# Optimization experiments

Hardware: AMD Instinct MI355X
Metric: run time of the kernel (lower is better)

Reference implementation:

```python
import jax, jax.numpy as jnp
import numpy as np

B, S, D, H, FF, V, L = 2, 2048, 1024, 16, 4096, 32000, 4
HD = D // H
SCALE = HD ** -0.5
STD = 0.02


def _ln(x, w, b, eps=1e-5):
    mu = jnp.mean(x, axis=-1, keepdims=True)
    var = jnp.mean(jnp.square(x - mu), axis=-1, keepdims=True)
    return (x - mu) * jax.lax.rsqrt(var + eps) * w + b


def setup_inputs() -> dict:
    key = jax.random.key(0)
    ks = iter(jax.random.split(key, 16))

    def w(k, shape):
        return jax.random.normal(k, shape, jnp.float32) * STD

    inp = {
        "tokens": jax.random.randint(next(ks), (B, S), 0, V, jnp.int32),
        "tok_emb": w(next(ks), (V, D)),
        "ln_e_w": jnp.ones((D,), jnp.float32),
        "ln_e_b": jnp.zeros((D,), jnp.float32),
        "ln1_w": jnp.ones((L, D), jnp.float32),
        "ln1_b": jnp.zeros((L, D), jnp.float32),
        "wq": w(next(ks), (L, D, D)),
        "bq": jnp.zeros((L, D), jnp.float32),
        "wk": w(next(ks), (L, D, D)),
        "bk": jnp.zeros((L, D), jnp.float32),
        "wv": w(next(ks), (L, D, D)),
        "bv": jnp.zeros((L, D), jnp.float32),
        "wo": w(next(ks), (L, D, D)),
        "bo": jnp.zeros((L, D), jnp.float32),
        "ln2_w": jnp.ones((L, D), jnp.float32),
        "ln2_b": jnp.zeros((L, D), jnp.float32),
        "w1": w(next(ks), (L, D, 2 * FF)),
        "b1": jnp.zeros((L, 2 * FF), jnp.float32),
        "w2": w(next(ks), (L, FF, D)),
        "b2": jnp.zeros((L, D), jnp.float32),
        "lnf_w": jnp.ones((D,), jnp.float32),
        "lnf_b": jnp.zeros((D,), jnp.float32),
        "w_out": w(next(ks), (D, V)),
        "b_out": jnp.zeros((V,), jnp.float32),
    }
    return inp


def reference(tokens, tok_emb, ln_e_w, ln_e_b, ln1_w, ln1_b, wq, bq, wk, bk,
              wv, bv, wo, bo, ln2_w, ln2_b, w1, b1, w2, b2, lnf_w, lnf_b,
              w_out, b_out):
    x = tok_emb[tokens]                      # [B,S,D]
    x = _ln(x, ln_e_w, ln_e_b)               # embedding LayerNorm (dropout off)
    for l in range(L):
        # pre-LN attention
        h = _ln(x, ln1_w[l], ln1_b[l])
        q = (h @ wq[l] + bq[l]).reshape(B, S, H, HD)
        k = (h @ wk[l] + bk[l]).reshape(B, S, H, HD)
        v = (h @ wv[l] + bv[l]).reshape(B, S, H, HD)
        scores = jnp.einsum('bqhd,bkhd->bhqk', q, k) * SCALE
        attn = jax.nn.softmax(scores, axis=-1)
        o = jnp.einsum('bhqk,bkhd->bqhd', attn, v).reshape(B, S, D)
        x = x + (o @ wo[l] + bo[l])
        # pre-LN gated (GeGLU) FFN
        h = _ln(x, ln2_w[l], ln2_b[l])
        gv = h @ w1[l] + b1[l]               # [B,S,2*FF]
        gate, val = gv[..., :FF], gv[..., FF:]
        ff = jax.nn.gelu(gate, approximate=False) * val
        x = x + (ff @ w2[l] + b2[l])
    x = _ln(x, lnf_w, lnf_b)
    return x @ w_out + b_out                 # logits [B,S,V]
```

## Files before the change

### kernel.cpp

```cpp
#include <hip/hip_runtime.h>

typedef __attribute__((ext_vector_type(8))) short s16x8;
typedef __attribute__((ext_vector_type(4))) short s16x4;
typedef __attribute__((ext_vector_type(4))) float f32x4;

__device__ __forceinline__ unsigned short f2bf(float f){
    union{float f;unsigned u;}v; v.f=f;
    unsigned u=v.u;
    unsigned r=(u+0x7fffu+((u>>16)&1u))>>16;
    return (unsigned short)r;
}
__device__ __forceinline__ float bf2f(unsigned short s){
    union{unsigned u;float f;}v; v.u=((unsigned)s)<<16; return v.f;
}
__device__ __forceinline__ unsigned pk2t(float a, float b){
    return (__float_as_uint(a)>>16) | (__float_as_uint(b) & 0xffff0000u);
}
__device__ __forceinline__ unsigned pk2r(float a, float b){
    return (unsigned)f2bf(a) | ((unsigned)f2bf(b)<<16);
}
__device__ __forceinline__ f32x4 fmax4(f32x4 a, f32x4 b){
    f32x4 r; r[0]=fmaxf(a[0],b[0]); r[1]=fmaxf(a[1],b[1]);
    r[2]=fmaxf(a[2],b[2]); r[3]=fmaxf(a[3],b[3]); return r;
}

__device__ __forceinline__ void gl16(const void* g, void* l){
    __builtin_amdgcn_global_load_lds(
        (const __attribute__((address_space(1))) void*)g,
        (__attribute__((address_space(3))) void*)l, 16, 0, 0);
}

#define ATT_SCALE 0.125f

__global__ __launch_bounds__(256) void flash_k(
    const unsigned short* __restrict__ qkv,
    const unsigned short* __restrict__ vt,
    unsigned short* __restrict__ o)
{
    __shared__ __align__(16) unsigned short Pl[4][2048];
    const int t=threadIdx.x, w=t>>6, lane=t&63;
    const int lr=lane&15, lg=lane>>4;
    const int zb=blockIdx.y>>4, zh=blockIdx.y&15;
    const long sr0 = (long)zb*2048 + blockIdx.x*128 + w*32;
    const unsigned short* qb    = qkv + sr0*3072 + zh*64;
    const unsigned short* kbase = qkv + ((long)zb*2048)*3072 + 1024 + zh*64;
    const unsigned short* vtb   = vt + (long)zb*2097152 + (long)zh*131072;

    s16x8 qf[2][2];
    #pragma unroll
    for(int qg=0;qg<2;qg++)
        #pragma unroll
        for(int kc=0;kc<2;kc++)
            qf[qg][kc] = *(const s16x8*)(qb + (qg*16+lr)*3072 + kc*32 + lg*8);

    float m0=-1e30f, m1=-1e30f, l0=0.f, l1=0.f;
    f32x4 oa[2][4];
    #pragma unroll
    for(int qg=0;qg<2;qg++)
        #pragma unroll
        for(int dt=0;dt<4;dt++) oa[qg][dt]=f32x4{0.f,0.f,0.f,0.f};

    char* Pw = (char*)&Pl[w][0];
    const int swz = (lr&7)<<4;

    for(int kv0=0; kv0<2048; kv0+=64){
        f32x4 s[2][4];
        __builtin_amdgcn_s_setprio(1);
        #pragma unroll
        for(int kb=0;kb<4;kb++){
            const unsigned short* kr = kbase + (long)(kv0+kb*16+lr)*3072;
            s16x8 a0 = *(const s16x8*)(kr + lg*8);
            s16x8 a1 = *(const s16x8*)(kr + 32 + lg*8);
            #pragma unroll
            for(int qg=0;qg<2;qg++){
                f32x4 z4{0.f,0.f,0.f,0.f};
                z4 = __builtin_amdgcn_mfma_f32_16x16x32_bf16(a0, qf[qg][0], z4,0,0,0);
                s[qg][kb] = __builtin_amdgcn_mfma_f32_16x16x32_bf16(a1, qf[qg][1], z4,0,0,0);
            }
        }
        __builtin_amdgcn_s_setprio(0);
        s16x8 vreg[4][2];
        #pragma unroll
        for(int dt=0;dt<4;dt++){
            const unsigned short* vr = vtb + (dt*16+lr)*2048 + kv0;
            vreg[dt][0] = *(const s16x8*)(vr + lg*8);
            vreg[dt][1] = *(const s16x8*)(vr + 32 + lg*8);
        }
        #pragma unroll
        for(int qg=0;qg<2;qg++){
            float& m = qg? m1:m0;
            float& l = qg? l1:l0;
            f32x4 mx4 = fmax4(fmax4(s[qg][0],s[qg][1]),fmax4(s[qg][2],s[qg][3]));
            float bm = fmaxf(fmaxf(mx4[0],mx4[1]),fmaxf(mx4[2],mx4[3]));
            bm = fmaxf(bm, __shfl_xor(bm,16));
            bm = fmaxf(bm, __shfl_xor(bm,32));
            const float mn = fmaxf(m, bm);
            const float sc = __expf((m-mn)*ATT_SCALE);
            m = mn;
            float rs=0.f;
            #pragma unroll
            for(int kb=0;kb<4;kb++){
                f32x4 p;
                #pragma unroll
                for(int r=0;r<4;r++){ p[r]=__expf((s[qg][kb][r]-mn)*ATT_SCALE); rs+=p[r]; }
                s[qg][kb]=p;
            }
            rs += __shfl_xor(rs,16);
            rs += __shfl_xor(rs,32);
            l = l*sc + rs;
            #pragma unroll
            for(int dt=0;dt<4;dt++) oa[qg][dt] = oa[qg][dt]*sc;
            #pragma unroll
            for(int kb=0;kb<4;kb++){
                uint2 pw;
                pw.x = pk2t(s[qg][kb][0], s[qg][kb][1]);
                pw.y = pk2t(s[qg][kb][2], s[qg][kb][3]);
                *(uint2*)(Pw + (qg*16+lr)*128 + ((kb*32+lg*8)^swz)) = pw;
            }
        }
        asm volatile("s_waitcnt lgkmcnt(0)" ::: "memory");
        s16x8 pb0[2], pb1[2];
        #pragma unroll
        for(int qg=0;qg<2;qg++){
            pb0[qg] = *(const s16x8*)(Pw + (qg*16+lr)*128 + ((     lg*16)^swz));
            pb1[qg] = *(const s16x8*)(Pw + (qg*16+lr)*128 + ((64 + lg*16)^swz));
        }
        __builtin_amdgcn_s_setprio(1);
        #pragma unroll
        for(int dt=0;dt<4;dt++){
            #pragma unroll
            for(int qg=0;qg<2;qg++){
                oa[qg][dt] = __builtin_amdgcn_mfma_f32_16x16x32_bf16(vreg[dt][0], pb0[qg], oa[qg][dt],0,0,0);
                oa[qg][dt] = __builtin_amdgcn_mfma_f32_16x16x32_bf16(vreg[dt][1], pb1[qg], oa[qg][dt],0,0,0);
            }
        }
        __builtin_amdgcn_s_setprio(0);
    }
    #pragma unroll
    for(int qg=0;qg<2;qg++){
        const float inv = 1.f/(qg? l1:l0);
        #pragma unroll
        for(int dt=0;dt<4;dt++){
            uint2 st;
            st.x = pk2r(oa[qg][dt][0]*inv, oa[qg][dt][1]*inv);
            st.y = pk2r(oa[qg][dt][2]*inv, oa[qg][dt][3]*inv);
            *(uint2*)(o + (sr0+qg*16+lr)*1024 + zh*64 + dt*16 + lg*4) = st;
        }
    }
}

template<bool OBF16,bool BIAS,bool GEGLU>
__global__ __launch_bounds__(512,2) void gemm8_k(
    const unsigned short* __restrict__ A,
    const unsigned short* __restrict__ B,
    const float* __restrict__ bias,
    void* __restrict__ Cp,
    int K,int lda,int ldb,int ldc)
{
    __shared__ __align__(16) char lds[131072];
    const int t=threadIdx.x, w=t>>6, lane=t&63;
    const int wr=w>>2, wc=w&3;
    const int lr=lane&15, lg=lane>>4;

    const int nwg = gridDim.x*gridDim.y;
    const int id  = blockIdx.y*gridDim.x + blockIdx.x;
    const int nid = (id&7)*(nwg>>3) + (id>>3);
    const long row0 = (long)(nid % gridDim.x)*256;
    const long col0 = (long)(nid / gridDim.x)*256;

    const int NT = K>>6;

    const int csw0 = (lg*16) ^ ((lr&7)<<4);
    const int aRow = (wr*64+lr)*128;
    const int bRow = (wc*32+lr)*128;

    const int sro = t>>3;
    const int sce = (((t&7) ^ ((t>>3)&7))<<3);

#define STAGE(gp, ld_, lb) do{ \
    const unsigned short* _g=(gp); char* _l=(lb); \
    gl16(_g + (long)sro*(ld_) + sce, _l + t*16); \
    gl16(_g + (long)(sro+64)*(ld_) + sce, _l + 8192 + t*16); }while(0)

#define LDA8(m,kk) (*(const s16x8*)(Ab_ + aRow + ((m)&3)*2048 + ((m)>>2)*16384 + ((kk)? (csw0^64):csw0)))
#define LDB8(n,kk) (*(const s16x8*)(Bb_ + bRow + ((n)&1)*2048 + ((n)>>1)*16384 + ((kk)? (csw0^64):csw0)))

    f32x4 acc[8][4];
    #pragma unroll
    for(int m=0;m<8;m++)
        #pragma unroll
        for(int n=0;n<4;n++) acc[m][n]=f32x4{0.f,0.f,0.f,0.f};

    STAGE(A + row0*lda,        lda, lds);
    STAGE(B + col0*ldb,        ldb, lds+65536);
    STAGE(A + (row0+128)*lda,  lda, lds+16384);
    STAGE(B + (col0+128)*ldb,  ldb, lds+65536+16384);
    STAGE(A + row0*lda + 64,   lda, lds+32768);
    STAGE(B + col0*ldb + 64,   ldb, lds+65536+32768);
    asm volatile("s_waitcnt vmcnt(4)" ::: "memory");
    __builtin_amdgcn_s_barrier();

    for(int tt=0; tt<NT; ++tt){
        char* Ab_ = lds + ((tt&1)<<15);
        char* Bb_ = lds + 65536 + ((tt&1)<<15);
        char* An  = lds + (((tt+1)&1)<<15);
        char* Bn  = lds + 65536 + (((tt+1)&1)<<15);
        const int k1=(tt+1)<<6, k2=(tt+2)<<6;
        s16x8 a[4][2], b01[2][2], b23[2][2];

        #pragma unroll
        for(int m=0;m<4;m++){ a[m][0]=LDA8(m,0); a[m][1]=LDA8(m,1); }
        #pragma unroll
        for(int n=0;n<2;n++){ b01[n][0]=LDB8(n,0); b01[n][1]=LDB8(n,1); }
        if(tt+1<NT) STAGE(A + (row0+128)*lda + k1, lda, An+16384);
        __builtin_amdgcn_s_barrier();
        __builtin_amdgcn_s_setprio(1);
        #pragma unroll
        for(int kk=0;kk<2;kk++)
            #pragma unroll
            for(int m=0;m<4;m++)
                #pragma unroll
                for(int n=0;n<2;n++)
                    acc[m][n]=__builtin_amdgcn_mfma_f32_16x16x32_bf16(a[m][kk],b01[n][kk],acc[m][n],0,0,0);
        __builtin_amdgcn_s_setprio(0);
        __builtin_amdgcn_s_barrier();

        #pragma unroll
        for(int n=0;n<2;n++){ b23[n][0]=LDB8(n+2,0); b23[n][1]=LDB8(n+2,1); }
        if(tt+1<NT) STAGE(B + (col0+128)*ldb + k1, ldb, Bn+16384);
        __builtin_amdgcn_s_barrier();
        __builtin_amdgcn_s_setprio(1);
        #pragma unroll
        for(int kk=0;kk<2;kk++)
            #pragma unroll
            for(int m=0;m<4;m++)
                #pragma unroll
                for(int n=0;n<2;n++)
                    acc[m][n+2]=__builtin_amdgcn_mfma_f32_16x16x32_bf16(a[m][kk],b23[n][kk],acc[m][n+2],0,0,0);
        __builtin_amdgcn_s_setprio(0);
        __builtin_amdgcn_s_barrier();

        #pragma unroll
        for(int m=0;m<4;m++){ a[m][0]=LDA8(m+4,0); a[m][1]=LDA8(m+4,1); }
        if(tt+2<NT) STAGE(A + row0*lda + k2, lda, Ab_);
        __builtin_amdgcn_s_barrier();
        __builtin_amdgcn_s_setprio(1);
        #pragma unroll
        for(int kk=0;kk<2;kk++)
            #pragma unroll
            for(int m=0;m<4;m++)
                #pragma unroll
                for(int n=0;n<2;n++)
                    acc[m+4][n]=__builtin_amdgcn_mfma_f32_16x16x32_bf16(a[m][kk],b01[n][kk],acc[m+4][n],0,0,0);
        __builtin_amdgcn_s_setprio(0);
        __builtin_amdgcn_s_barrier();

        if(tt+2<NT) STAGE(B + col0*ldb + k2, ldb, Bb_);
        __builtin_amdgcn_s_barrier();
        __builtin_amdgcn_s_setprio(1);
        #pragma unroll
        for(int kk=0;kk<2;kk++)
            #pragma unroll
            for(int m=0;m<4;m++)
                #pragma unroll
                for(int n=0;n<2;n++)
                    acc[m+4][n+2]=__builtin_amdgcn_mfma_f32_16x16x32_bf16(a[m][kk],b23[n][kk],acc[m+4][n+2],0,0,0);
        __builtin_amdgcn_s_setprio(0);
        if(tt+2<NT) asm volatile("s_waitcnt vmcnt(4)" ::: "memory");
        else        asm volatile("s_waitcnt vmcnt(0)" ::: "memory");
        __builtin_amdgcn_s_barrier();
    }

    if constexpr(GEGLU){
        const long hc0 = col0>>1;
        #pragma unroll
        for(int m=0;m<8;m++){
            #pragma unroll
            for(int n=0;n<2;n++){
                #pragma unroll
                for(int rr=0;rr<4;rr++){
                    const long grow = row0 + wr*64 + (m&3)*16 + (m>>2)*128 + lg*4 + rr;
                    const long g    = hc0 + wc*32 + n*16 + lr;
                    float gg = acc[m][n][rr]   + bias[g];
                    float vl = acc[m][n+2][rr] + bias[4096+g];
                    float ge = 0.5f*gg*(1.f+erff(gg*0.70710678118654752f));
                    ((unsigned short*)Cp)[grow*(long)ldc + g] = f2bf(ge*vl);
                }
            }
        }
    } else if constexpr(!OBF16){
        float* L = (float*)lds;
        const int lc4 = (t&63)*4;
        f32x4 bv{0.f,0.f,0.f,0.f};
        if constexpr(BIAS) bv = *(const f32x4*)(bias + col0 + lc4);
        #pragma unroll
        for(int ch=0; ch<2; ch++){
            __builtin_amdgcn_s_barrier();
            #pragma unroll
            for(int mm=0;mm<4;mm++){
                #pragma unroll
                for(int n=0;n<4;n++){
                    #pragma unroll
                    for(int rr=0;rr<4;rr++){
                        const int lrow = wr*64 + mm*16 + lg*4 + rr;
                        const int lcol = wc*32 + (n&1)*16 + (n>>1)*128 + lr;
                        L[lrow*256 + lcol] = acc[ch*4+mm][n][rr];
                    }
                }
            }
            __builtin_amdgcn_s_barrier();
            #pragma unroll
            for(int p=0;p<16;p++){
                const int lrow = p*8 + (t>>6);
                f32x4 v4 = *(const f32x4*)(L + lrow*256 + lc4);
                if constexpr(BIAS){ v4[0]+=bv[0]; v4[1]+=bv[1]; v4[2]+=bv[2]; v4[3]+=bv[3]; }
                *(f32x4*)((float*)Cp + (row0 + ch*128 + lrow)*(long)ldc + col0 + lc4) = v4;
            }
        }
    } else {
        #pragma unroll
        for(int m=0;m<8;m++){
            #pragma unroll
            for(int n=0;n<4;n++){
                #pragma unroll
                for(int rr=0;rr<4;rr++){
                    const long grow = row0 + wr*64 + (m&3)*16 + (m>>2)*128 + lg*4 + rr;
                    const long gcol = col0 + wc*32 + (n&1)*16 + (n>>1)*128 + lr;
                    float vv = acc[m][n][rr];
                    if constexpr(BIAS) vv += bias[gcol];
                    ((unsigned short*)Cp)[grow*(long)ldc+gcol]=f2bf(vv);
                }
            }
        }
    }
#undef STAGE
#undef LDA8
#undef LDB8
}

__global__ __launch_bounds__(256) void cat3_k(const float* __restrict__ a,
    const float* __restrict__ b, const float* __restrict__ c,
    float* __restrict__ out)
{
    const int i = blockIdx.x*256+threadIdx.x;
    const int l = i/3072, cc = i%3072;
    float v = (cc<1024)? a[l*1024+cc] : (cc<2048)? b[l*1024+cc-1024] : c[l*1024+cc-2048];
    out[i]=v;
}

template<int BM,int BN,int WN,bool BIAS,bool RES,bool OBF16,bool SCL,bool SWAP,bool GEGLU>
__global__ __launch_bounds__(256) void gemm_bt(
    const unsigned short* __restrict__ A,
    const unsigned short* __restrict__ B,
    const unsigned short* __restrict__ B2,
    const float* __restrict__ bias,
    const float* __restrict__ res,
    void* __restrict__ Cp,
    int K,int lda,int ldb,int ldc,
    long aSb,long aSh,long bSb,long bSh,long cSb,long cSh,int zH)
{
    constexpr int BK=64;
    constexpr int WM=4/WN, WTM=BM/WM, WTN=BN/WN;
    constexpr int FM=WTM/16, FN=WTN/16;
    constexpr int CA=BM/8, CB=BN/8;
    __shared__ __align__(16) unsigned short As[BM*BK];
    __shared__ __align__(16) unsigned short Bs[BN*BK*(GEGLU?2:1)];

    const int t=threadIdx.x, w=t>>6, lane=t&63;
    const int wr=w/WN, wc=w%WN;
    const int lr=lane&15, lg=lane>>4;
    const int z=blockIdx.z, zb=z/zH, zh=z%zH;
    const long row0 = SWAP ? (long)blockIdx.x*BM : (long)blockIdx.y*BM;
    const long col0 = SWAP ? (long)blockIdx.y*BN : (long)blockIdx.x*BN;

    const unsigned short* Ab = A + zb*aSb + zh*aSh;
    const unsigned short* Bb = B + zb*bSb + zh*bSh;

    const int lr8 = lane>>3;
    const int lc8 = (lane&7)<<3;

    f32x4 acc[FM][FN];
    f32x4 acc2[GEGLU?FM:1][GEGLU?FN:1];
    #pragma unroll
    for(int i=0;i<FM;i++)
        #pragma unroll
        for(int j=0;j<FN;j++){
            acc[i][j]=f32x4{0.f,0.f,0.f,0.f};
            if constexpr(GEGLU) acc2[i][j]=f32x4{0.f,0.f,0.f,0.f};
        }

    const int NT=K/BK;
    for(int kt=0;kt<NT;kt++){
        const int kb=kt*BK;
        #pragma unroll
        for(int cc=0;cc<CA/4;cc++){
            const int c=cc*4+w;
            gl16(Ab + (row0 + c*8 + lr8)*(long)lda + kb + lc8, (char*)As + c*1024);
        }
        #pragma unroll
        for(int cc=0;cc<CB/4;cc++){
            const int c=cc*4+w;
            gl16(Bb + (col0 + c*8 + lr8)*(long)ldb + kb + lc8, (char*)Bs + c*1024);
        }
        if constexpr(GEGLU){
            #pragma unroll
            for(int cc=0;cc<CB/4;cc++){
                const int c=cc*4+w;
                gl16(B2 + (col0 + c*8 + lr8)*(long)ldb + kb + lc8,
                     (char*)Bs + (CB + c)*1024);
            }
        }
        __syncthreads();
        const unsigned short* Arp = As + (wr*WTM+lr)*BK + lg*8;
        const unsigned short* Brp = Bs + (wc*WTN+lr)*BK + lg*8;
        #pragma unroll
        for(int kk=0;kk<2;kk++){
            s16x8 af[FM], bfv[FN], bf2[GEGLU?FN:1];
            #pragma unroll
            for(int i=0;i<FM;i++) af[i] = *(const s16x8*)(Arp + i*16*BK + kk*32);
            #pragma unroll
            for(int j=0;j<FN;j++) bfv[j]= *(const s16x8*)(Brp + j*16*BK + kk*32);
            if constexpr(GEGLU){
                #pragma unroll
                for(int j=0;j<FN;j++) bf2[j]=*(const s16x8*)(Brp + BN*BK + j*16*BK + kk*32);
            }
            #pragma unroll
            for(int i=0;i<FM;i++)
                #pragma unroll
                for(int j=0;j<FN;j++){
                    acc[i][j]=__builtin_amdgcn_mfma_f32_16x16x32_bf16(af[i],bfv[j],acc[i][j],0,0,0);
                    if constexpr(GEGLU)
                        acc2[i][j]=__builtin_amdgcn_mfma_f32_16x16x32_bf16(af[i],bf2[j],acc2[i][j],0,0,0);
                }
        }
        __syncthreads();
    }
    #pragma unroll
    for(int i=0;i<FM;i++){
        #pragma unroll
        for(int j=0;j<FN;j++){
            #pragma unroll
            for(int r=0;r<4;r++){
                const long grow = row0 + wr*WTM + i*16 + lg*4 + r;
                const long gcol = col0 + wc*WTN + j*16 + lr;
                if constexpr(GEGLU){
                    float g  = acc[i][j][r]  + bias[gcol];
                    float vl = acc2[i][j][r] + bias[gcol+4096];
                    float ge = 0.5f*g*(1.f+erff(g*0.70710678118654752f));
                    ((unsigned short*)Cp)[grow*ldc+gcol] = f2bf(ge*vl);
                } else {
                    float vv=acc[i][j][r];
                    if constexpr(SCL)  vv*=ATT_SCALE;
                    if constexpr(BIAS) vv+=bias[gcol];
                    if constexpr(RES)  vv+=res[grow*ldc+gcol];
                    const long cidx = zb*cSb + zh*cSh + grow*ldc + gcol;
                    if constexpr(OBF16) ((unsigned short*)Cp)[cidx]=f2bf(vv);
                    else                ((float*)Cp)[cidx]=vv;
                }
            }
        }
    }
}

template<bool IN32, bool REMAP>
__global__ __launch_bounds__(256) void tr_k(const void* __restrict__ in,
    unsigned short* __restrict__ out, int ldin, int ldout,
    long inZb, long inZh, long outZb, long outZh, int zH)
{
    __shared__ unsigned short tl[64][68];
    const int t=threadIdx.x;
    const int z=blockIdx.z, zb=z/zH, zh=z%zH;
    const long ib=(long)blockIdx.x*64*ldin + (long)blockIdx.y*64 + zb*inZb + zh*inZh;
    long orow = (long)blockIdx.y*64;
    if constexpr(REMAP){
        orow = (orow < 4096) ? ((orow>>7)*256 + (orow&127))
                             : (((orow-4096)>>7)*256 + 128 + ((orow-4096)&127));
    }
    const long ob=orow*ldout + (long)blockIdx.x*64 + zb*outZb + zh*outZh;
    const int r0=t>>4, c0=(t&15)*4;
    #pragma unroll
    for(int p=0;p<4;p++){
        const int rr=r0+p*16;
        if constexpr(IN32){
            f32x4 v=*(const f32x4*)((const float*)in + ib + (long)rr*ldin + c0);
            #pragma unroll
            for(int i=0;i<4;i++) tl[c0+i][rr]=f2bf(v[i]);
        } else {
            s16x4 v=*(const s16x4*)((const unsigned short*)in + ib + (long)rr*ldin + c0);
            #pragma unroll
            for(int i=0;i<4;i++) tl[c0+i][rr]=(unsigned short)v[i];
        }
    }
    __syncthreads();
    #pragma unroll
    for(int p=0;p<4;p++){
        const int rr=r0+p*16;
        s16x4 o4;
        #pragma unroll
        for(int i=0;i<4;i++) o4[i]=(short)tl[rr][c0+i];
        *(s16x4*)(out + ob + (long)rr*ldout + c0)=o4;
    }
}

template<bool GATHER, bool OBF16>
__global__ __launch_bounds__(256) void ln_k(const float* __restrict__ in,
    const float* __restrict__ w, const float* __restrict__ b,
    void* __restrict__ out, const int* __restrict__ tok)
{
    const int row = blockIdx.x, t = threadIdx.x;
    const float* src;
    if constexpr (GATHER) src = in + (long)tok[row]*1024;
    else                  src = in + (long)row*1024;
    const int c = t*4;
    f32x4 xv = *(const f32x4*)(src + c);
    float s  = xv[0]+xv[1]+xv[2]+xv[3];
    float qq = xv[0]*xv[0]+xv[1]*xv[1]+xv[2]*xv[2]+xv[3]*xv[3];
    #pragma unroll
    for(int m=32;m;m>>=1){ s += __shfl_xor(s,m); qq += __shfl_xor(qq,m); }
    __shared__ float rs_[4], rq_[4];
    if((t&63)==0){ rs_[t>>6]=s; rq_[t>>6]=qq; }
    __syncthreads();
    s  = rs_[0]+rs_[1]+rs_[2]+rs_[3];
    qq = rq_[0]+rq_[1]+rq_[2]+rq_[3];
    const float mu = s*(1.f/1024.f);
    const float rstd = rsqrtf(qq*(1.f/1024.f)-mu*mu + 1e-5f);
    f32x4 wv = *(const f32x4*)(w+c), bv = *(const f32x4*)(b+c);
    if constexpr (OBF16){
        s16x4 ov;
        #pragma unroll
        for(int i=0;i<4;i++) ov[i]=(short)f2bf((xv[i]-mu)*rstd*wv[i]+bv[i]);
        *(s16x4*)((unsigned short*)out + (long)row*1024 + c) = ov;
    } else {
        f32x4 ov;
        #pragma unroll
        for(int i=0;i<4;i++) ov[i]=(xv[i]-mu)*rstd*wv[i]+bv[i];
        *(f32x4*)((float*)out + (long)row*1024 + c) = ov;
    }
}

template<int BM,int BN,int WN,bool BIAS>
__global__ __launch_bounds__(256) void gemm_k(
    const unsigned short* __restrict__ A,
    const float* __restrict__ Bp,
    const float* __restrict__ bias,
    float* __restrict__ Cp,
    int K,int lda,int ldb,int ldc)
{
    constexpr int BK=64, PAD=24, LDS_=BK+PAD;
    constexpr int WM = 4/WN;
    constexpr int WTM = BM/WM, WTN = BN/WN;
    constexpr int FM = WTM/16, FN = WTN/16;
    __shared__ unsigned short As[BM*LDS_];
    __shared__ unsigned short Bs[BN*LDS_];

    const int t = threadIdx.x;
    const int w = t>>6, lane = t&63;
    const int wr = w / WN, wc = w % WN;
    const int lr = lane & 15, lg = lane >> 4;

    const long row0 = (long)blockIdx.y*BM;
    const long col0 = (long)blockIdx.x*BN;

    f32x4 acc[FM][FN];
    #pragma unroll
    for(int i=0;i<FM;i++)
        #pragma unroll
        for(int j=0;j<FN;j++) acc[i][j] = f32x4{0.f,0.f,0.f,0.f};

    const int NT = K/BK;
    for(int kt=0; kt<NT; ++kt){
        const int kb = kt*BK;
        {
            constexpr int PASS = BM*BK/(256*4);
            #pragma unroll
            for(int p=0;p<PASS;p++){
                int idx = (p*256+t)*4;
                int r = idx/BK, c = idx%BK;
                *(s16x4*)&As[r*LDS_+c] = *(const s16x4*)(A + (row0+r)*lda + kb + c);
            }
        }
        {
            constexpr int TPB = 256/BN;
            constexpr int KC  = BK/TPB;
            const int n = t % BN, k0 = (t/BN)*KC;
            #pragma unroll
            for(int j0=0;j0<KC;j0+=8){
                s16x8 pk;
                #pragma unroll
                for(int i=0;i<8;i++){
                    const long gk = (long)kb + k0 + j0 + i;
                    pk[i] = (short)f2bf(Bp[gk*ldb + col0 + n]);
                }
                *(s16x8*)&Bs[n*LDS_ + k0 + j0] = pk;
            }
        }
        __syncthreads();
        const unsigned short* Ar = &As[(wr*WTM + lr)*LDS_ + lg*8];
        const unsigned short* Br = &Bs[(wc*WTN + lr)*LDS_ + lg*8];
        #pragma unroll
        for(int kk=0;kk<BK/32;kk++){
            s16x8 af[FM], bfv[FN];
            #pragma unroll
            for(int i=0;i<FM;i++) af[i]  = *(const s16x8*)(Ar + i*16*LDS_ + kk*32);
            #pragma unroll
            for(int j=0;j<FN;j++) bfv[j] = *(const s16x8*)(Br + j*16*LDS_ + kk*32);
            #pragma unroll
            for(int i=0;i<FM;i++)
                #pragma unroll
                for(int j=0;j<FN;j++)
                    acc[i][j] = __builtin_amdgcn_mfma_f32_16x16x32_bf16(af[i],bfv[j],acc[i][j],0,0,0);
        }
        __syncthreads();
    }
    #pragma unroll
    for(int i=0;i<FM;i++){
        #pragma unroll
        for(int j=0;j<FN;j++){
            #pragma unroll
            for(int r=0;r<4;r++){
                long grow = row0 + wr*WTM + i*16 + lg*4 + r;
                long gcol = col0 + wc*WTN + j*16 + lr;
                float vv = acc[i][j][r];
                if constexpr (BIAS) vv += bias[gcol];
                Cp[grow*ldc + gcol] = vv;
            }
        }
    }
}

extern "C" void kernel_launch(void* const* d_in, const int* in_sizes, int n_in,
                              void* d_out, int out_size, void* d_ws, size_t ws_size,
                              hipStream_t stream)
{
    const int*   tokens  = (const int*)  d_in[0];
    const float* tok_emb = (const float*)d_in[1];
    const float* ln_e_w  = (const float*)d_in[2];
    const float* ln_e_b  = (const float*)d_in[3];
    const float* ln1_w   = (const float*)d_in[4];
    const float* ln1_b   = (const float*)d_in[5];
    const float* wq      = (const float*)d_in[6];
    const float* bq      = (const float*)d_in[7];
    const float* wk      = (const float*)d_in[8];
    const float* bk      = (const float*)d_in[9];
    const float* wv      = (const float*)d_in[10];
    const float* bv      = (const float*)d_in[11];
    const float* wo      = (const float*)d_in[12];
    const float* bo      = (const float*)d_in[13];
    const float* ln2_w   = (const float*)d_in[14];
    const float* ln2_b   = (const float*)d_in[15];
    const float* w1      = (const float*)d_in[16];
    const float* b1      = (const float*)d_in[17];
    const float* w2      = (const float*)d_in[18];
    const float* b2      = (const float*)d_in[19];
    const float* lnf_w   = (const float*)d_in[20];
    const float* lnf_b   = (const float*)d_in[21];
    const float* w_out   = (const float*)d_in[22];
    const float* b_out   = (const float*)d_in[23];

    const int D=1024;
    const long DD  = (long)D*D;
    const long WQKV_L = 3145728L;

    unsigned short *wqkvT,*woT,*w1T,*w2T,*woutT=nullptr;
    float *x,*bqkv;
    unsigned short *h,*qkv,*vt,*o,*ff;
    bool fastTier;
    if (ws_size >= 301989888ull){
        char* p=(char*)d_ws;
        wqkvT=(unsigned short*)(p);
        woT  =(unsigned short*)(p+25165824);
        w1T  =(unsigned short*)(p+33554432);
        w2T  =(unsigned short*)(p+100663296);
        woutT=(unsigned short*)(p+134217728);
        x    =(float*)(p+201326592);
        h    =(unsigned short*)(p+218103808);
        qkv  =(unsigned short*)(p+226492416);
        vt   =(unsigned short*)(p+251658240);
        o    =(unsigned short*)(p+260046848);
        ff   =(unsigned short*)(p+268435456);
        bqkv =(float*)((char*)d_out + 134217728);
        fastTier=true;
    } else {
        char* p=(char*)d_out;
        qkv  =(unsigned short*)(p);
        bqkv =(float*)(p+25165824);
        wqkvT=(unsigned short*)(p+268435456);
        woT  =(unsigned short*)(p+293601280);
        w1T  =(unsigned short*)(p+301989888);
        w2T  =(unsigned short*)(p+369098752);
        x    =(float*)(p+402653184);
        vt   =(unsigned short*)(p+444596224);
        o    =(unsigned short*)(p+452984832);
        ff   =(unsigned short*)(p+461373440);
        h    =(unsigned short*)d_ws;
        fastTier=false;
    }

    const dim3 blk(256,1,1), blk8(512,1,1);

    tr_k<true,false><<<dim3(16,16,4), blk,0,stream>>>(wq, wqkvT,         1024,1024, DD,0, WQKV_L,0, 1);
    tr_k<true,false><<<dim3(16,16,4), blk,0,stream>>>(wk, wqkvT+1048576, 1024,1024, DD,0, WQKV_L,0, 1);
    tr_k<true,false><<<dim3(16,16,4), blk,0,stream>>>(wv, wqkvT+2097152, 1024,1024, DD,0, WQKV_L,0, 1);
    tr_k<true,false><<<dim3(16,16,4), blk,0,stream>>>(wo, woT, 1024,1024, DD,0, DD,0, 1);
    if (fastTier){
        tr_k<true,true><<<dim3(16,128,4),blk,0,stream>>>(w1, w1T, 8192,1024, 8388608L,0, 8388608L,0, 1);
        tr_k<true,false><<<dim3(16,500,1),blk,0,stream>>>(w_out, woutT, 32000,1024, 0,0, 0,0, 1);
    } else {
        tr_k<true,false><<<dim3(16,128,4),blk,0,stream>>>(w1, w1T, 8192,1024, 8388608L,0, 8388608L,0, 1);
    }
    tr_k<true,false><<<dim3(64,16,4), blk,0,stream>>>(w2, w2T, 1024,4096, 4194304L,0, 4194304L,0, 1);
    cat3_k<<<48,blk,0,stream>>>(bq, bk, bv, bqkv);

    ln_k<true,false><<<4096,blk,0,stream>>>(tok_emb, ln_e_w, ln_e_b, x, tokens);

    const dim3 g_d(8,32,1);

    for(int l=0;l<4;l++){
        ln_k<false,true><<<4096,blk,0,stream>>>(x, ln1_w+l*D, ln1_b+l*D, h, nullptr);
        gemm8_k<true,true,false><<<dim3(16,12,1),blk8,0,stream>>>(
            h, wqkvT+l*WQKV_L, bqkv+l*3072, qkv, 1024, 1024,1024,3072);
        tr_k<false,false><<<dim3(32,1,32),blk,0,stream>>>(qkv+2048, vt, 3072,2048,
            2048L*3072,64, 2097152L,131072L, 16);
        flash_k<<<dim3(16,32,1),blk,0,stream>>>(qkv, vt, o);
        gemm_bt<128,128,2,true,true,false,false,false,false><<<g_d,blk,0,stream>>>(
            o, woT+l*DD, nullptr, bo+l*D, x, x, 1024, 1024,1024,1024, 0,0,0,0,0,0, 1);
        ln_k<false,true><<<4096,blk,0,stream>>>(x, ln2_w+l*D, ln2_b+l*D, h, nullptr);
        if (fastTier){
            gemm8_k<true,true,true><<<dim3(16,32,1),blk8,0,stream>>>(
                h, w1T+l*8388608L, b1+(long)l*8192, ff, 1024, 1024,1024,4096);
        } else {
            gemm_bt<128,64,1,true,false,true,false,false,true><<<dim3(64,32,1),blk,0,stream>>>(
                h, w1T+l*8388608L, w1T+l*8388608L+4194304L, b1+(long)l*8192, nullptr, ff,
                1024, 1024,1024,4096, 0,0,0,0,0,0, 1);
        }
        gemm_bt<128,128,2,true,true,false,false,false,false><<<g_d,blk,0,stream>>>(
            ff, w2T+l*4194304L, nullptr, b2+l*D, x, x, 4096, 4096,4096,1024, 0,0,0,0,0,0, 1);
    }

    ln_k<false,true><<<4096,blk,0,stream>>>(x, lnf_w, lnf_b, h, nullptr);

    if (fastTier){
        gemm8_k<false,true,false><<<dim3(16,125,1),blk8,0,stream>>>(
            h, woutT, b_out, (float*)d_out, 1024, 1024,1024,32000);
    } else {
        gemm_k<128,128,2,true><<<dim3(250,32,1),blk,0,stream>>>(
            h, w_out, b_out, (float*)d_out, 1024, 1024,32000,32000);
    }
}
```

Baseline: 1.998 ms.

## Merge GEMM main loop into two phases, swizzle epilogue LDS, widen transpose

The 256x256 GEMM main loop drops from four MFMA phases per K-step to two. All four B fragments are loaded at once, and both the A and B staging loads are issued together in each phase, so there are fewer barriers and the global loads are grouped. The fp32 epilogue XOR-swizzles its LDS staging to avoid bank conflicts and writes the output with nontemporal stores. The transpose kernel moves to 8-element vector loads and stores with a smaller padded tile. The trade-off is higher register pressure from holding all B fragments at once, and a change in how loads overlap with compute.

```diff
diff --git a/kernel.cpp b/kernel.cpp
--- a/kernel.cpp
+++ b/kernel.cpp
@@ -206,13 +206,16 @@
         char* An  = lds + (((tt+1)&1)<<15);
         char* Bn  = lds + 65536 + (((tt+1)&1)<<15);
         const int k1=(tt+1)<<6, k2=(tt+2)<<6;
-        s16x8 a[4][2], b01[2][2], b23[2][2];
+        s16x8 a[4][2], b[4][2];
 
         #pragma unroll
         for(int m=0;m<4;m++){ a[m][0]=LDA8(m,0); a[m][1]=LDA8(m,1); }
         #pragma unroll
-        for(int n=0;n<2;n++){ b01[n][0]=LDB8(n,0); b01[n][1]=LDB8(n,1); }
-        if(tt+1<NT) STAGE(A + (row0+128)*lda + k1, lda, An+16384);
+        for(int n=0;n<4;n++){ b[n][0]=LDB8(n,0); b[n][1]=LDB8(n,1); }
+        if(tt+1<NT){
+            STAGE(A + (row0+128)*lda + k1, lda, An+16384);
+            STAGE(B + (col0+128)*ldb + k1, ldb, Bn+16384);
+        }
         __builtin_amdgcn_s_barrier();
         __builtin_amdgcn_s_setprio(1);
         #pragma unroll
@@ -220,14 +223,17 @@
             #pragma unroll
             for(int m=0;m<4;m++)
                 #pragma unroll
-                for(int n=0;n<2;n++)
-                    acc[m][n]=__builtin_amdgcn_mfma_f32_16x16x32_bf16(a[m][kk],b01[n][kk],acc[m][n],0,0,0);
+                for(int n=0;n<4;n++)
+                    acc[m][n]=__builtin_amdgcn_mfma_f32_16x16x32_bf16(a[m][kk],b[n][kk],acc[m][n],0,0,0);
         __builtin_amdgcn_s_setprio(0);
         __builtin_amdgcn_s_barrier();
 
         #pragma unroll
-        for(int n=0;n<2;n++){ b23[n][0]=LDB8(n+2,0); b23[n][1]=LDB8(n+2,1); }
-        if(tt+1<NT) STAGE(B + (col0+128)*ldb + k1, ldb, Bn+16384);
+        for(int m=0;m<4;m++){ a[m][0]=LDA8(m+4,0); a[m][1]=LDA8(m+4,1); }
+        if(tt+2<NT){
+            STAGE(A + row0*lda + k2, lda, Ab_);
+            STAGE(B + col0*ldb + k2, ldb, Bb_);
+        }
         __builtin_amdgcn_s_barrier();
         __builtin_amdgcn_s_setprio(1);
         #pragma unroll
@@ -235,36 +241,8 @@
             #pragma unroll
             for(int m=0;m<4;m++)
                 #pragma unroll
-                for(int n=0;n<2;n++)
-                    acc[m][n+2]=__builtin_amdgcn_mfma_f32_16x16x32_bf16(a[m][kk],b23[n][kk],acc[m][n+2],0,0,0);
-        __builtin_amdgcn_s_setprio(0);
-        __builtin_amdgcn_s_barrier();
-
-        #pragma unroll
-        for(int m=0;m<4;m++){ a[m][0]=LDA8(m+4,0); a[m][1]=LDA8(m+4,1); }
-        if(tt+2<NT) STAGE(A + row0*lda + k2, lda, Ab_);
-        __builtin_amdgcn_s_barrier();
-        __builtin_amdgcn_s_setprio(1);
-        #pragma unroll
-        for(int kk=0;kk<2;kk++)
-            #pragma unroll
-            for(int m=0;m<4;m++)
-                #pragma unroll
-                for(int n=0;n<2;n++)
-                    acc[m+4][n]=__builtin_amdgcn_mfma_f32_16x16x32_bf16(a[m][kk],b01[n][kk],acc[m+4][n],0,0,0);
-        __builtin_amdgcn_s_setprio(0);
-        __builtin_amdgcn_s_barrier();
-
-        if(tt+2<NT) STAGE(B + col0*ldb + k2, ldb, Bb_);
-        __builtin_amdgcn_s_barrier();
-        __builtin_amdgcn_s_setprio(1);
-        #pragma unroll
-        for(int kk=0;kk<2;kk++)
-            #pragma unroll
-            for(int m=0;m<4;m++)
-                #pragma unroll
-                for(int n=0;n<2;n++)
-                    acc[m+4][n+2]=__builtin_amdgcn_mfma_f32_16x16x32_bf16(a[m][kk],b23[n][kk],acc[m+4][n+2],0,0,0);
+                for(int n=0;n<4;n++)
+                    acc[m+4][n]=__builtin_amdgcn_mfma_f32_16x16x32_bf16(a[m][kk],b[n][kk],acc[m+4][n],0,0,0);
         __builtin_amdgcn_s_setprio(0);
         if(tt+2<NT) asm volatile("s_waitcnt vmcnt(4)" ::: "memory");
         else        asm volatile("s_waitcnt vmcnt(0)" ::: "memory");
@@ -290,7 +268,7 @@
         }
     } else if constexpr(!OBF16){
         float* L = (float*)lds;
-        const int lc4 = (t&63)*4;
+        const int lc4 = (t&63)<<2;
         f32x4 bv{0.f,0.f,0.f,0.f};
         if constexpr(BIAS) bv = *(const f32x4*)(bias + col0 + lc4);
         #pragma unroll
@@ -304,7 +282,8 @@
                     for(int rr=0;rr<4;rr++){
                         const int lrow = wr*64 + mm*16 + lg*4 + rr;
                         const int lcol = wc*32 + (n&1)*16 + (n>>1)*128 + lr;
-                        L[lrow*256 + lcol] = acc[ch*4+mm][n][rr];
+                        const int pc = ((((lcol>>2) ^ (lrow&7))<<2) | (lcol&3));
+                        L[lrow*256 + pc] = acc[ch*4+mm][n][rr];
                     }
                 }
             }
@@ -312,9 +291,11 @@
             #pragma unroll
             for(int p=0;p<16;p++){
                 const int lrow = p*8 + (t>>6);
-                f32x4 v4 = *(const f32x4*)(L + lrow*256 + lc4);
+                const int pc4 = (((lc4>>2) ^ (lrow&7))<<2);
+                f32x4 v4 = *(const f32x4*)(L + lrow*256 + pc4);
                 if constexpr(BIAS){ v4[0]+=bv[0]; v4[1]+=bv[1]; v4[2]+=bv[2]; v4[3]+=bv[3]; }
-                *(f32x4*)((float*)Cp + (row0 + ch*128 + lrow)*(long)ldc + col0 + lc4) = v4;
+                __builtin_nontemporal_store(v4,
+                    (f32x4*)((float*)Cp + (row0 + ch*128 + lrow)*(long)ldc + col0 + lc4));
             }
         }
     } else {
@@ -467,7 +448,7 @@
     unsigned short* __restrict__ out, int ldin, int ldout,
     long inZb, long inZh, long outZb, long outZh, int zH)
 {
-    __shared__ unsigned short tl[64][68];
+    __shared__ unsigned short tl[64][66];
     const int t=threadIdx.x;
     const int z=blockIdx.z, zb=z/zH, zh=z%zH;
     const long ib=(long)blockIdx.x*64*ldin + (long)blockIdx.y*64 + zb*inZb + zh*inZh;
@@ -477,28 +458,29 @@
                              : (((orow-4096)>>7)*256 + 128 + ((orow-4096)&127));
     }
     const long ob=orow*ldout + (long)blockIdx.x*64 + zb*outZb + zh*outZh;
-    const int r0=t>>4, c0=(t&15)*4;
-    #pragma unroll
-    for(int p=0;p<4;p++){
-        const int rr=r0+p*16;
+    const int r0=t>>3, c8=(t&7)*8;
+    #pragma unroll
+    for(int p=0;p<2;p++){
+        const int rr=r0+p*32;
         if constexpr(IN32){
-            f32x4 v=*(const f32x4*)((const float*)in + ib + (long)rr*ldin + c0);
-            #pragma unroll
-            for(int i=0;i<4;i++) tl[c0+i][rr]=f2bf(v[i]);
+            f32x4 v0=*(const f32x4*)((const float*)in + ib + (long)rr*ldin + c8);
+            f32x4 v1=*(const f32x4*)((const float*)in + ib + (long)rr*ldin + c8+4);
+            #pragma unroll
+            for(int i=0;i<4;i++){ tl[c8+i][rr]=f2bf(v0[i]); tl[c8+4+i][rr]=f2bf(v1[i]); }
         } else {
-            s16x4 v=*(const s16x4*)((const unsigned short*)in + ib + (long)rr*ldin + c0);
-            #pragma unroll
-            for(int i=0;i<4;i++) tl[c0+i][rr]=(unsigned short)v[i];
+            s16x8 v=*(const s16x8*)((const unsigned short*)in + ib + (long)rr*ldin + c8);
+            #pragma unroll
+            for(int i=0;i<8;i++) tl[c8+i][rr]=(unsigned short)v[i];
         }
     }
     __syncthreads();
     #pragma unroll
-    for(int p=0;p<4;p++){
-        const int rr=r0+p*16;
-        s16x4 o4;
-        #pragma unroll
-        for(int i=0;i<4;i++) o4[i]=(short)tl[rr][c0+i];
-        *(s16x4*)(out + ob + (long)rr*ldout + c0)=o4;
+    for(int p=0;p<2;p++){
+        const int rr=r0+p*32;
+        s16x8 o8;
+        #pragma unroll
+        for(int i=0;i<8;i++) o8[i]=(short)tl[rr][c8+i];
+        *(s16x8*)(out + ob + (long)rr*ldout + c8)=o8;
     }
 }
 
```

Measured after the change: 1.956 ms. 2.1% less time.
